# Performance work log

Measured on AMD Instinct MI355X. Metric: run time of the kernel, lower is better.

## Reference

```python
import jax, jax.numpy as jnp
import numpy as np

DIM = 1024
NUM_HEADS = 16
HEAD_DIM = DIM // NUM_HEADS


def setup_inputs() -> dict:
    key = jax.random.key(0)
    k1, k2, k3 = jax.random.split(key, 3)
    B, T = 2, 2048
    x = jax.random.normal(k1, (B, T, DIM), dtype=jnp.float32)
    # qkv: Linear(dim, 3*dim, bias=False); torch weight shape [3*dim, dim]
    w_qkv = jax.random.normal(k2, (3 * DIM, DIM), dtype=jnp.float32) * (1.0 / np.sqrt(DIM))
    # out_proj: Linear(dim, dim, bias=False) (zeros in orig init; random for a meaningful baseline)
    w_out = jax.random.normal(k3, (DIM, DIM), dtype=jnp.float32) * (1.0 / np.sqrt(DIM))
    return {"x": x, "w_qkv": w_qkv, "w_out": w_out}


def reference(x, w_qkv, w_out):
    B, T, C = x.shape
    H, D = NUM_HEADS, HEAD_DIM
    qkv = jnp.einsum("btc,fc->btf", x, w_qkv)            # [B,T,3C]
    qkv = qkv.reshape(B, T, 3, H, D).transpose(2, 0, 3, 1, 4)  # [3,B,H,T,D]
    q, k, v = qkv[0], qkv[1], qkv[2]
    scale = 1.0 / np.sqrt(D)
    scores = jnp.einsum("bhtd,bhsd->bhts", q, k) * scale  # [B,H,T,T]
    causal = jnp.tril(jnp.ones((T, T), dtype=bool))
    scores = jnp.where(causal, scores, -jnp.inf)
    attn = jax.nn.softmax(scores, axis=-1)
    out = jnp.einsum("bhts,bhsd->bhtd", attn, v)          # [B,H,T,D]
    out = out.transpose(0, 2, 1, 3).reshape(B, T, C)       # [B,T,C]
    return jnp.einsum("btc,oc->bto", out, w_out)
```

## Files before the change

kernel.cpp:

```cpp
#include <hip/hip_runtime.h>
#include <hip/hip_bf16.h>

typedef __attribute__((ext_vector_type(8))) short vbf8;
typedef __attribute__((ext_vector_type(4))) float vf4;
typedef __attribute__((ext_vector_type(4))) unsigned int vu4;

#define MFMA16(a, b, c) __builtin_amdgcn_mfma_f32_16x16x32_bf16((a), (b), (c), 0, 0, 0)

__device__ __forceinline__ unsigned short f2bf(float f) {
    unsigned int u = __float_as_uint(f);
    u += 0x7fffu + ((u >> 16) & 1u);
    return (unsigned short)(u >> 16);
}

__device__ __forceinline__ void gload_lds16(const void* g, void* l) {
    __builtin_amdgcn_global_load_lds(
        (const __attribute__((address_space(1))) unsigned int*)(unsigned long long)g,
        (__attribute__((address_space(3))) unsigned int*)(unsigned long long)l,
        16, 0, 0);
}

__global__ __launch_bounds__(256) void cvt_all(
    const float* __restrict__ x, const float* __restrict__ wq, const float* __restrict__ wo,
    unsigned short* __restrict__ xb, unsigned short* __restrict__ wqb, unsigned short* __restrict__ wob)
{
    int i = blockIdx.x * 256 + threadIdx.x;
    const float* src;
    unsigned short* dst;
    int off;
    if (i < 1048576)      { src = x;  dst = xb;  off = i; }
    else if (i < 1835008) { src = wq; dst = wqb; off = i - 1048576; }
    else                  { src = wo; dst = wob; off = i - 1835008; }
    float4 v = ((const float4*)src)[off];
    ushort4 o;
    o.x = f2bf(v.x); o.y = f2bf(v.y); o.z = f2bf(v.z); o.w = f2bf(v.w);
    ((ushort4*)dst)[off] = o;
}

template <int EPI>
__global__ __launch_bounds__(256) void gemm_bt(
    const unsigned short* __restrict__ A, const unsigned short* __restrict__ Bt,
    int M, int N, int K,
    float* __restrict__ Cf,
    unsigned short* __restrict__ Qo, unsigned short* __restrict__ Ko, unsigned short* __restrict__ Vo)
{
    __shared__ __align__(16) unsigned short sA[128 * 64];
    __shared__ __align__(16) unsigned short sB[128 * 64];

    const int tid = threadIdx.x;
    const int lane = tid & 63;
    const int w = tid >> 6;
    const int wr = w >> 1, wc = w & 1;
    const int l16 = lane & 15, lhi = lane >> 4;
    const int bm = blockIdx.y, bn = blockIdx.x;
    const int row0 = bm * 128, col0 = bn * 128;

    vf4 acc[4][4] = {};

    for (int k0 = 0; k0 < K; k0 += 64) {
#pragma unroll
        for (int i = 0; i < 4; ++i) {
            int p = i * 256 + tid;
            int r = p >> 3, cb = p & 7;
            int cs = cb ^ (r & 7);
            gload_lds16(A + (size_t)(row0 + r) * K + k0 + (cs << 3), &sA[p << 3]);
            gload_lds16(Bt + (size_t)(col0 + r) * K + k0 + (cs << 3), &sB[p << 3]);
        }
        __syncthreads();
#pragma unroll
        for (int kk = 0; kk < 2; ++kk) {
            const int cb = kk * 4 + lhi;
            vbf8 af[4], bfr[4];
#pragma unroll
            for (int mt = 0; mt < 4; ++mt) {
                int r = wr * 64 + mt * 16 + l16;
                af[mt] = *(const vbf8*)&sA[(r << 6) + ((cb ^ (r & 7)) << 3)];
            }
#pragma unroll
            for (int nt = 0; nt < 4; ++nt) {
                int r = wc * 64 + nt * 16 + l16;
                bfr[nt] = *(const vbf8*)&sB[(r << 6) + ((cb ^ (r & 7)) << 3)];
            }
#pragma unroll
            for (int mt = 0; mt < 4; ++mt)
#pragma unroll
                for (int nt = 0; nt < 4; ++nt)
                    acc[mt][nt] = MFMA16(af[mt], bfr[nt], acc[mt][nt]);
        }
        __syncthreads();
    }

#pragma unroll
    for (int mt = 0; mt < 4; ++mt) {
#pragma unroll
        for (int nt = 0; nt < 4; ++nt) {
#pragma unroll
            for (int r = 0; r < 4; ++r) {
                int row = row0 + wr * 64 + mt * 16 + lhi * 4 + r;
                int col = col0 + wc * 64 + nt * 16 + l16;
                float v = acc[mt][nt][r];
                if (EPI == 0) {
                    Cf[(size_t)row * N + col] = v;
                } else {
                    int which = col >> 10, rem = col & 1023;
                    int h = rem >> 6, d = rem & 63;
                    int b = row >> 11, t = row & 2047;
                    size_t bh = (size_t)(b * 16 + h);
                    if (which == 0)      Qo[(bh * 2048 + t) * 64 + d] = f2bf(v * 0.125f);
                    else if (which == 1) Ko[(bh * 2048 + t) * 64 + d] = f2bf(v);
                    else                 Vo[(bh * 64 + d) * 2048 + t] = f2bf(v);
                }
            }
        }
    }
}

__global__ __launch_bounds__(512, 4) void attn_fwd3(
    const unsigned short* __restrict__ Q, const unsigned short* __restrict__ Kp,
    const unsigned short* __restrict__ Vt, unsigned short* __restrict__ att)
{
    __shared__ __align__(16) unsigned short sK[2][128 * 64];
    __shared__ __align__(16) unsigned short sV[2][64 * 128];

    const int tid = threadIdx.x;
    const int lane = tid & 63;
    const int w = tid >> 6;
    const int l16 = lane & 15, lhi = lane >> 4;
    const int bh = blockIdx.x & 31;
    const int band = 15 - (blockIdx.x >> 5);
    const size_t hoff = (size_t)bh * 2048 * 64;
    const unsigned short* Qh = Q + hoff;
    const unsigned short* Kh = Kp + hoff;
    const unsigned short* Vh = Vt + hoff;
    const int q0 = band * 128;
    const int qg = q0 + w * 16 + l16;
    const int ktLast = band;

    const int pA = tid, pB = 512 + tid;
    const int rKA = pA >> 3, cKA = pA & 7;
    const int rKB = pB >> 3, cKB = pB & 7;
    const int rVA = pA >> 4, cVA = pA & 15;
    const int rVB = pB >> 4, cVB = pB & 15;
    const unsigned short* pKA = Kh + (size_t)rKA * 64 + ((cKA ^ (rKA & 7)) << 3);
    const unsigned short* pKB = Kh + (size_t)rKB * 64 + ((cKB ^ (rKB & 7)) << 3);
    const unsigned short* pVA = Vh + (size_t)rVA * 2048 + ((cVA ^ (rVA & 7)) << 3);
    const unsigned short* pVB = Vh + (size_t)rVB * 2048 + ((cVB ^ (rVB & 7)) << 3);
    const int dA = pA << 3, dB = pB << 3;

    auto STAGE = [&](int buf, int k0) {
        gload_lds16(pKA + (size_t)k0 * 64, &sK[buf][dA]);
        gload_lds16(pKB + (size_t)k0 * 64, &sK[buf][dB]);
        gload_lds16(pVA + k0, &sV[buf][dA]);
        gload_lds16(pVB + k0, &sV[buf][dB]);
    };

    STAGE(0, 0);

    vbf8 qf[2];
#pragma unroll
    for (int kk = 0; kk < 2; ++kk)
        qf[kk] = *(const vbf8*)&Qh[(size_t)qg * 64 + kk * 32 + lhi * 8];

    vf4 oacc[4] = {};
    float m = -1e30f, lsum = 0.f;

    for (int kt = 0; kt <= ktLast; ++kt) {
        const int cur = kt & 1;
        const int k0 = kt * 128;
        if (kt < ktLast) {
            STAGE(cur ^ 1, k0 + 128);
            asm volatile("s_waitcnt vmcnt(4)" ::: "memory");
        } else {
            asm volatile("s_waitcnt vmcnt(0)" ::: "memory");
        }
        __builtin_amdgcn_s_barrier();
        __builtin_amdgcn_sched_barrier(0);

        const unsigned short* sKc = &sK[cur][0];
        const unsigned short* sVc = &sV[cur][0];

        vf4 sc[8] = {};
#pragma unroll
        for (int kk = 0; kk < 2; ++kk) {
#pragma unroll
            for (int nt = 0; nt < 8; ++nt) {
                int rr = nt * 16 + l16;
                vbf8 kf = *(const vbf8*)&sKc[(rr << 6) + ((((kk << 2) + lhi) ^ (rr & 7)) << 3)];
                sc[nt] = MFMA16(kf, qf[kk], sc[nt]);
            }
        }

        if (kt == ktLast) {
#pragma unroll
            for (int nt = 0; nt < 8; ++nt)
#pragma unroll
                for (int r = 0; r < 4; ++r) {
                    int kg = k0 + nt * 16 + lhi * 4 + r;
                    if (kg > qg) sc[nt][r] = -1e30f;
                }
        }

        float pm = -1e30f;
#pragma unroll
        for (int nt = 0; nt < 8; ++nt)
#pragma unroll
            for (int r = 0; r < 4; ++r) pm = fmaxf(pm, sc[nt][r]);
        pm = fmaxf(pm, __shfl_xor(pm, 16, 64));
        pm = fmaxf(pm, __shfl_xor(pm, 32, 64));
        float mn = fmaxf(m, pm);
        float alpha = __expf(m - mn);
        m = mn;
        float rs = 0.f;
#pragma unroll
        for (int nt = 0; nt < 8; ++nt)
#pragma unroll
            for (int r = 0; r < 4; ++r) {
                float p = __expf(sc[nt][r] - mn);
                sc[nt][r] = p;
                rs += p;
            }
        rs += __shfl_xor(rs, 16, 64);
        rs += __shfl_xor(rs, 32, 64);
        lsum = lsum * alpha + rs;
#pragma unroll
        for (int dt = 0; dt < 4; ++dt)
#pragma unroll
            for (int r = 0; r < 4; ++r) oacc[dt][r] *= alpha;

        unsigned int pk0[8], pk1[8];
#pragma unroll
        for (int nt = 0; nt < 8; ++nt) {
            pk0[nt] = (unsigned int)f2bf(sc[nt][0]) | ((unsigned int)f2bf(sc[nt][1]) << 16);
            pk1[nt] = (unsigned int)f2bf(sc[nt][2]) | ((unsigned int)f2bf(sc[nt][3]) << 16);
        }

        const int srcA = l16 + ((lhi & 1) ? 32 : 0);
        const int srcB = srcA + 16;
        const bool hiSel = (lhi >> 1) != 0;
#pragma unroll
        for (int kk = 0; kk < 4; ++kk) {
            unsigned int a0e = __shfl((int)pk0[2 * kk], srcA, 64);
            unsigned int a1e = __shfl((int)pk1[2 * kk], srcA, 64);
            unsigned int b0e = __shfl((int)pk0[2 * kk], srcB, 64);
            unsigned int b1e = __shfl((int)pk1[2 * kk], srcB, 64);
            unsigned int a0o = __shfl((int)pk0[2 * kk + 1], srcA, 64);
            unsigned int a1o = __shfl((int)pk1[2 * kk + 1], srcA, 64);
            unsigned int b0o = __shfl((int)pk0[2 * kk + 1], srcB, 64);
            unsigned int b1o = __shfl((int)pk1[2 * kk + 1], srcB, 64);
            vu4 uw;
            uw.x = hiSel ? a0o : a0e;
            uw.y = hiSel ? a1o : a1e;
            uw.z = hiSel ? b0o : b0e;
            uw.w = hiSel ? b1o : b1e;
            vbf8 pf = __builtin_bit_cast(vbf8, uw);
#pragma unroll
            for (int dt = 0; dt < 4; ++dt) {
                int rr = dt * 16 + l16;
                vbf8 vfr = *(const vbf8*)&sVc[(rr << 7) + ((((kk << 2) + lhi) ^ (rr & 7)) << 3)];
                oacc[dt] = MFMA16(vfr, pf, oacc[dt]);
            }
        }
        __builtin_amdgcn_s_barrier();
        __builtin_amdgcn_sched_barrier(0);
    }

    const float inv = 1.0f / lsum;
    unsigned short* so = &sK[0][0] + w * 1024;
#pragma unroll
    for (int dt = 0; dt < 4; ++dt)
#pragma unroll
        for (int r = 0; r < 4; ++r)
            so[l16 * 64 + (((dt * 2 + (lhi >> 1)) ^ (l16 & 7)) << 3) + (lhi & 1) * 4 + r] =
                f2bf(oacc[dt][r] * inv);
    __syncthreads();

    const int b = bh >> 4, h = bh & 15;
    const int qr = lane >> 2;
    const int cj = lane & 3;
    vbf8 o1 = *(const vbf8*)&so[qr * 64 + (((cj * 2 + 0) ^ (qr & 7)) << 3)];
    vbf8 o2 = *(const vbf8*)&so[qr * 64 + (((cj * 2 + 1) ^ (qr & 7)) << 3)];
    const int qrow = q0 + w * 16 + qr;
    unsigned short* dst = att + ((size_t)(b * 2048 + qrow)) * 1024 + h * 64 + cj * 16;
    *(vbf8*)dst = o1;
    *(vbf8*)(dst + 8) = o2;
}

extern "C" void kernel_launch(void* const* d_in, const int* in_sizes, int n_in,
                              void* d_out, int out_size, void* d_ws, size_t ws_size,
                              hipStream_t stream) {
    const float* x = (const float*)d_in[0];
    const float* w_qkv = (const float*)d_in[1];
    const float* w_out = (const float*)d_in[2];
    float* out = (float*)d_out;

    char* ws = (char*)d_ws;
    unsigned short* xb   = (unsigned short*)(ws);
    unsigned short* wqb  = (unsigned short*)(ws + (8ull << 20));
    unsigned short* wob  = (unsigned short*)(ws + (14ull << 20));
    unsigned short* Qb   = (unsigned short*)(ws + (16ull << 20));
    unsigned short* Kb   = (unsigned short*)(ws + (24ull << 20));
    unsigned short* Vb   = (unsigned short*)(ws + (32ull << 20));
    unsigned short* attb = (unsigned short*)(ws + (40ull << 20));

    cvt_all<<<8192, 256, 0, stream>>>(x, w_qkv, w_out, xb, wqb, wob);

    gemm_bt<1><<<dim3(3072 / 128, 4096 / 128), 256, 0, stream>>>(
        xb, wqb, 4096, 3072, 1024, nullptr, Qb, Kb, Vb);

    attn_fwd3<<<16 * 32, 512, 0, stream>>>(Qb, Kb, Vb, attb);

    gemm_bt<0><<<dim3(1024 / 128, 4096 / 128), 256, 0, stream>>>(
        attb, wob, 4096, 1024, 1024, out, nullptr, nullptr, nullptr);
}
```

Measured before the change: 124.1 us.

## Use exp2 softmax with lazy rescale, packed bf16 convert, and balanced band order

Folds log2(e) into the Q scale so the softmax can use exp2f, and skips the running-max rescale of the output accumulator unless some lane's max grows by more than 8. It also swaps software bf16 rounding for the packed hardware convert instruction, tree-reduces the max and sum, and reorders the causal query bands so heavy and light blocks interleave. The aim is fewer VALU ops per tile and less tail imbalance. Lazy rescaling lets probabilities exceed 1 (up to 2^8), which costs some bf16 precision.

After: 118.4 us. -4.6%, faster.

```diff
diff --git a/kernel.cpp b/kernel.cpp
--- a/kernel.cpp
+++ b/kernel.cpp
@@ -11,6 +11,12 @@
     unsigned int u = __float_as_uint(f);
     u += 0x7fffu + ((u >> 16) & 1u);
     return (unsigned short)(u >> 16);
+}
+
+__device__ __forceinline__ unsigned int cvtpk(float a, float b) {
+    unsigned int r;
+    asm("v_cvt_pk_bf16_f32 %0, %1, %2" : "=v"(r) : "v"(a), "v"(b));
+    return r;
 }
 
 __device__ __forceinline__ void gload_lds16(const void* g, void* l) {
@@ -106,7 +112,7 @@
                     int h = rem >> 6, d = rem & 63;
                     int b = row >> 11, t = row & 2047;
                     size_t bh = (size_t)(b * 16 + h);
-                    if (which == 0)      Qo[(bh * 2048 + t) * 64 + d] = f2bf(v * 0.125f);
+                    if (which == 0)      Qo[(bh * 2048 + t) * 64 + d] = f2bf(v * 0.18033688011112042f);
                     else if (which == 1) Ko[(bh * 2048 + t) * 64 + d] = f2bf(v);
                     else                 Vo[(bh * 64 + d) * 2048 + t] = f2bf(v);
                 }
@@ -115,7 +121,7 @@
     }
 }
 
-__global__ __launch_bounds__(512, 4) void attn_fwd3(
+__global__ __launch_bounds__(512, 4) void attn_fwd4(
     const unsigned short* __restrict__ Q, const unsigned short* __restrict__ Kp,
     const unsigned short* __restrict__ Vt, unsigned short* __restrict__ att)
 {
@@ -127,7 +133,8 @@
     const int w = tid >> 6;
     const int l16 = lane & 15, lhi = lane >> 4;
     const int bh = blockIdx.x & 31;
-    const int band = 15 - (blockIdx.x >> 5);
+    const int j = blockIdx.x >> 5;
+    const int band = (j < 8) ? (15 - j) : (j - 8);
     const size_t hoff = (size_t)bh * 2048 * 64;
     const unsigned short* Qh = Q + hoff;
     const unsigned short* Kh = Kp + hoff;
@@ -200,38 +207,44 @@
                 }
         }
 
-        float pm = -1e30f;
+        float m4[8];
 #pragma unroll
         for (int nt = 0; nt < 8; ++nt)
-#pragma unroll
-            for (int r = 0; r < 4; ++r) pm = fmaxf(pm, sc[nt][r]);
+            m4[nt] = fmaxf(fmaxf(sc[nt][0], sc[nt][1]), fmaxf(sc[nt][2], sc[nt][3]));
+        float pm = fmaxf(fmaxf(fmaxf(m4[0], m4[1]), fmaxf(m4[2], m4[3])),
+                         fmaxf(fmaxf(m4[4], m4[5]), fmaxf(m4[6], m4[7])));
         pm = fmaxf(pm, __shfl_xor(pm, 16, 64));
         pm = fmaxf(pm, __shfl_xor(pm, 32, 64));
-        float mn = fmaxf(m, pm);
-        float alpha = __expf(m - mn);
-        m = mn;
-        float rs = 0.f;
-#pragma unroll
-        for (int nt = 0; nt < 8; ++nt)
-#pragma unroll
-            for (int r = 0; r < 4; ++r) {
-                float p = __expf(sc[nt][r] - mn);
-                sc[nt][r] = p;
-                rs += p;
-            }
+
+        if (!__all(pm - m <= 8.0f)) {
+            float mn = fmaxf(m, pm);
+            float alpha = exp2f(m - mn);
+            lsum *= alpha;
+#pragma unroll
+            for (int dt = 0; dt < 4; ++dt)
+#pragma unroll
+                for (int r = 0; r < 4; ++r) oacc[dt][r] *= alpha;
+            m = mn;
+        }
+
+        float rs4[8];
+#pragma unroll
+        for (int nt = 0; nt < 8; ++nt) {
+#pragma unroll
+            for (int r = 0; r < 4; ++r) sc[nt][r] = exp2f(sc[nt][r] - m);
+            rs4[nt] = (sc[nt][0] + sc[nt][1]) + (sc[nt][2] + sc[nt][3]);
+        }
+        float rs = ((rs4[0] + rs4[1]) + (rs4[2] + rs4[3])) +
+                   ((rs4[4] + rs4[5]) + (rs4[6] + rs4[7]));
         rs += __shfl_xor(rs, 16, 64);
         rs += __shfl_xor(rs, 32, 64);
-        lsum = lsum * alpha + rs;
-#pragma unroll
-        for (int dt = 0; dt < 4; ++dt)
-#pragma unroll
-            for (int r = 0; r < 4; ++r) oacc[dt][r] *= alpha;
+        lsum += rs;
 
         unsigned int pk0[8], pk1[8];
 #pragma unroll
         for (int nt = 0; nt < 8; ++nt) {
-            pk0[nt] = (unsigned int)f2bf(sc[nt][0]) | ((unsigned int)f2bf(sc[nt][1]) << 16);
-            pk1[nt] = (unsigned int)f2bf(sc[nt][2]) | ((unsigned int)f2bf(sc[nt][3]) << 16);
+            pk0[nt] = cvtpk(sc[nt][0], sc[nt][1]);
+            pk1[nt] = cvtpk(sc[nt][2], sc[nt][3]);
         }
 
         const int srcA = l16 + ((lhi & 1) ? 32 : 0);
@@ -307,7 +320,7 @@
     gemm_bt<1><<<dim3(3072 / 128, 4096 / 128), 256, 0, stream>>>(
         xb, wqb, 4096, 3072, 1024, nullptr, Qb, Kb, Vb);
 
-    attn_fwd3<<<16 * 32, 512, 0, stream>>>(Qb, Kb, Vb, attb);
+    attn_fwd4<<<16 * 32, 512, 0, stream>>>(Qb, Kb, Vb, attb);
 
     gemm_bt<0><<<dim3(1024 / 128, 4096 / 128), 256, 0, stream>>>(
         attb, wob, 4096, 1024, 1024, out, nullptr, nullptr, nullptr);
```
